# Performance work log

Hardware: AMD Instinct MI355X
Metric: run time of the kernel (lower is better)

The kernel has to match this reference:

```python
import jax, jax.numpy as jnp
import numpy as np

B, SR, D, H, L, NH, ND, E, RK = 64, 29, 768, 3072, 12, 12, 14, 15, 8
S = SR + 1            # cls token + regions
SCALE = 16.0 / 8.0    # lora_alpha / lora_r
NE = L // 2           # number of even (MoE) layers


def _ln(x, g, b, eps):
    m = x.mean(-1, keepdims=True)
    v = ((x - m) ** 2).mean(-1, keepdims=True)
    return (x - m) * jax.lax.rsqrt(v + eps) * g + b


def _ln_plain(x, eps):
    # F.layer_norm with no affine params (expert output norm)
    m = x.mean(-1, keepdims=True)
    v = ((x - m) ** 2).mean(-1, keepdims=True)
    return (x - m) * jax.lax.rsqrt(v + eps)


def _mha(x, Wq, bq, Wk, bk, Wv, bv, Wo, bo):
    b_, s_, _ = x.shape
    dh = D // NH
    q = (x @ Wq.T + bq).reshape(b_, s_, NH, dh)
    k = (x @ Wk.T + bk).reshape(b_, s_, NH, dh)
    v = (x @ Wv.T + bv).reshape(b_, s_, NH, dh)
    att = jax.nn.softmax(jnp.einsum('bqhd,bkhd->bhqk', q, k) / np.float32(np.sqrt(dh)), axis=-1)
    o = jnp.einsum('bhqk,bkhd->bqhd', att, v).reshape(b_, s_, D)
    return o @ Wo.T + bo


def _forward(region_features, mask, cls_token, ln1_g, ln1_b, ln2_g, ln2_b,
             Wq, bq, Wk, bk, Wv, bv, Wao, bao, Wi, bi, Wo, bo, fg, fb,
             cW1, cb1, clng, clnb, cW2, cb2, A_up, B_up, A_down, B_down):
    bsz = region_features.shape[0]
    h = jnp.concatenate([jnp.broadcast_to(cls_token, (bsz, 1, D)), region_features], axis=1)
    col_counts = mask.sum(axis=0)  # [ND], guaranteed > 0 by construction
    for i in range(L):
        n1 = _ln(h, ln1_g[i], ln1_b[i], 1e-12)
        attn = _mha(n1, Wq[i], bq[i], Wk[i], bk[i], Wv[i], bv[i], Wao[i], bao[i])
        res1 = attn + h
        n2 = _ln(res1, ln2_g[i], ln2_b[i], 1e-12)
        inter = jax.nn.gelu(n2 @ Wi[i].T + bi[i], approximate=False)   # [B,S,H]
        base = inter @ Wo[i].T + bo[i]                                  # [B,S,D]
        if i % 2 == 0:
            e = i // 2
            # disease classifier: mask-gather region attention features, mean-pool, per-disease MLP
            region = attn[:, 1:, :]                                     # [B,SR,D]
            pooled = jnp.einsum('rd,brh->bdh', mask, region) / col_counts[None, :, None]
            z = jnp.einsum('bdh,dkh->bdk', pooled, cW1[e]) + cb1[e]
            z = jax.nn.gelu(_ln(z, clng[e], clnb[e], 1e-5), approximate=False)
            preds = jnp.einsum('bdk,dk->bd', z, cW2[e]) + cb2[e]        # [B,ND]
            disease_active = (jax.nn.sigmoid(preds) > 0.5).astype(h.dtype)
            # expert activation: general expert always on; disease experts per region-disease mask
            active = jnp.zeros((bsz, S, E), h.dtype).at[:, :, -1].set(1.0)
            region_active = disease_active[:, None, :] * mask[None, :, :]  # [B,SR,ND]
            active = active.at[:, 1:1 + SR, :ND].set(region_active)
            weights = active / jnp.maximum(active.sum(-1, keepdims=True), 1.0)
            # all 15 LoRA experts densely; zero-weight experts contribute nothing
            lup = jnp.einsum('bser,ehr->bseh', jnp.einsum('bsd,erd->bser', n2, A_up[e]), B_up[e]) * SCALE
            hid = inter[:, :, None, :] + lup                             # [B,S,E,H]
            ldown = jnp.einsum('bser,edr->bsed', jnp.einsum('bseh,erh->bser', hid, A_down[e]), B_down[e]) * SCALE
            out_e = _ln_plain(base[:, :, None, :] + ldown, 1e-5)         # [B,S,E,D]
            ffn_out = jnp.einsum('bsed,bse->bsd', out_e, weights)
        else:
            ffn_out = base
        h = ffn_out + res1
    return _ln(h, fg, fb, 1e-12)


def setup_inputs() -> dict:
    key = jax.random.key(0)
    ks = iter(jax.random.split(key, 64))
    p = lambda *sh: 0.02 * jax.random.normal(next(ks), sh, dtype=jnp.float32)
    g = lambda *sh: 1.0 + 0.02 * jax.random.normal(next(ks), sh, dtype=jnp.float32)
    return dict(
        region_features=jax.random.normal(next(ks), (B, SR, D), dtype=jnp.float32),
        mask=jax.random.bernoulli(next(ks), 0.5, (SR, ND)).astype(jnp.float32).at[0, :].set(1.0),
        cls_token=p(1, 1, D),
        ln1_g=g(L, D), ln1_b=p(L, D), ln2_g=g(L, D), ln2_b=p(L, D),
        Wq=p(L, D, D), bq=p(L, D), Wk=p(L, D, D), bk=p(L, D),
        Wv=p(L, D, D), bv=p(L, D), Wao=p(L, D, D), bao=p(L, D),
        Wi=p(L, H, D), bi=p(L, H), Wo=p(L, D, H), bo=p(L, D),
        fg=g(D), fb=p(D),
        cW1=p(NE, ND, D // 2, D), cb1=p(NE, ND, D // 2),
        clng=g(NE, ND, D // 2), clnb=p(NE, ND, D // 2),
        cW2=p(NE, ND, D // 2), cb2=p(NE, ND),
        A_up=p(NE, E, RK, D), B_up=p(NE, E, H, RK),
        A_down=p(NE, E, RK, H), B_down=p(NE, E, D, RK),
    )


def reference(region_features, mask, cls_token, ln1_g, ln1_b, ln2_g, ln2_b,
              Wq, bq, Wk, bk, Wv, bv, Wao, bao, Wi, bi, Wo, bo, fg, fb,
              cW1, cb1, clng, clnb, cW2, cb2, A_up, B_up, A_down, B_down):
    return _forward(region_features, mask, cls_token, ln1_g, ln1_b, ln2_g, ln2_b,
                    Wq, bq, Wk, bk, Wv, bv, Wao, bao, Wi, bi, Wo, bo, fg, fb,
                    cW1, cb1, clng, clnb, cW2, cb2, A_up, B_up, A_down, B_down)
```

## Files before the change

### kernel.cpp

```cpp
#include <hip/hip_runtime.h>

namespace {

constexpr int kB = 64, kSR = 29, kS = 30, kD = 768, kH = 3072, kL = 12;
constexpr int kNH = 12, kND = 14, kE = 15, kNE = 6;
constexpr int kRows = kB * kS;
constexpr int kQKV = 2304;

typedef __attribute__((ext_vector_type(8))) short s16x8;
typedef __attribute__((ext_vector_type(4))) float fx4;

__device__ __forceinline__ float gelu_f(float x) {
  return 0.5f * x * (1.0f + erff(x * 0.70710678118654752f));
}

__device__ __forceinline__ unsigned short f2bf_u(float x) {
  union { float f; unsigned u; } v;
  v.f = x;
  unsigned r = v.u + 0x7fffu + ((v.u >> 16) & 1u);
  return (unsigned short)(r >> 16);
}
__device__ __forceinline__ float bfu2f(unsigned short h) {
  union { unsigned u; float f; } v;
  v.u = ((unsigned)h) << 16;
  return v.f;
}

__device__ __forceinline__ void g2l16(const short* g, short* l) {
  __builtin_amdgcn_global_load_lds(
      (const __attribute__((address_space(1))) unsigned int*)g,
      (__attribute__((address_space(3))) unsigned int*)l, 16, 0, 0);
}

template <int N>
__device__ __forceinline__ void waitcnt_vm() {
  if constexpr (N == 0)
    asm volatile("s_waitcnt vmcnt(0)" ::: "memory");
  else if constexpr (N == 4)
    asm volatile("s_waitcnt vmcnt(4)" ::: "memory");
  else if constexpr (N == 6)
    asm volatile("s_waitcnt vmcnt(6)" ::: "memory");
  else
    asm volatile("s_waitcnt vmcnt(8)" ::: "memory");
  __builtin_amdgcn_sched_barrier(0);
}

__device__ __forceinline__ void swz_block(int& bx, int& by, int& bz) {
  int gx = gridDim.x, gy = gridDim.y;
  int nwg = gx * gy * (int)gridDim.z;
  int orig = blockIdx.x + gx * (blockIdx.y + gy * blockIdx.z);
  int q = nwg >> 3, r = nwg & 7;
  int xcd = orig & 7, idx = orig >> 3;
  int s = (xcd < r ? xcd * (q + 1) : r * (q + 1) + (xcd - r) * q) + idx;
  bx = s % gx;
  int t2 = s / gx;
  by = t2 % gy;
  bz = t2 / gy;
}

__device__ __forceinline__ float block_sum(float v) {
  __shared__ float sb[4];
#pragma unroll
  for (int o = 32; o > 0; o >>= 1) v += __shfl_down(v, o, 64);
  int w = threadIdx.x >> 6;
  __syncthreads();
  if ((threadIdx.x & 63) == 0) sb[w] = v;
  __syncthreads();
  return sb[0] + sb[1] + sb[2] + sb[3];
}

__device__ __forceinline__ float dot8(const float* __restrict__ p,
                                      const float* __restrict__ q) {
  float4 x = *(const float4*)p;
  float4 y = *(const float4*)(p + 4);
  return x.x * q[0] + x.y * q[1] + x.z * q[2] + x.w * q[3] +
         y.x * q[4] + y.y * q[5] + y.z * q[6] + y.w * q[7];
}

template <int BM, int BN, int MODE>
__global__ __launch_bounds__(256) void gemm_hl(
    const short* __restrict__ Ah, const short* __restrict__ Al,
    const short* __restrict__ Bh, const short* __restrict__ Bl,
    const float* __restrict__ bias, float* __restrict__ Cf,
    short* __restrict__ Ch, short* __restrict__ Cl, int K, int ldc, int act,
    int kchunk, long bsA, long bsB, long bsBias, long bsC) {
  constexpr int MFR = BM / 16, NFR = BN / 16;
  constexpr int NA = 2 * MFR, NB = 2 * NFR, LPW = (NA + NB) / 4;
  constexpr int MF_W = MFR / 2, NF_W = NFR / 2;
  constexpr int ABUF = 2 * MFR * 512, BBUF = 2 * NFR * 512;
  __shared__ __align__(16) short As[3][2][MFR][512];
  __shared__ __align__(16) short Bs[3][2][NFR][512];
  int bx, by, bz;
  swz_block(bx, by, bz);
  const int t = threadIdx.x, w = t >> 6, lane = t & 63;
  const int lr = lane & 15, lg = lane >> 4;
  const int m0 = by * BM, n0 = bx * BN;
  const int kst = K >> 5;
  int k0 = 0;
  if (MODE == 1) k0 = bz * kchunk;
  if (MODE == 2) {
    Ah += bz * bsA;
    Al += bz * bsA;
    Bh += bz * bsB;
    Bl += bz * bsB;
    if (bias) bias += bz * bsBias;
    Cf += bz * bsC;
  }
  const int nsteps = (MODE == 1 ? kchunk : K) >> 5;
  const int wmf = (w & 1) * MF_W, wnf = (w >> 1) * NF_W;

  const short* gp[LPW];
  short* lp[LPW];
  int bo[LPW], adv[LPW];
#pragma unroll
  for (int q = 0; q < LPW; q++) {
    int f = w * LPW + q;
    if (f < NA) {
      int p = f & 1, mf = f >> 1;
      gp[q] = (p ? Al : Ah) + (size_t)(m0 + mf * 16 + lr) * K + k0 + lg * 8;
      lp[q] = &As[0][p][mf][0];
      bo[q] = ABUF;
      adv[q] = 32;
    } else {
      int fb = f - NA, p = fb & 1, nf = fb >> 1;
      gp[q] = (p ? Bl : Bh) + ((size_t)(n0 / 16 + nf) * kst + (k0 >> 5)) * 512 +
              lane * 8;
      lp[q] = &Bs[0][p][nf][0];
      bo[q] = BBUF;
      adv[q] = 512;
    }
  }

  auto stage = [&](int bufidx) {
#pragma unroll
    for (int q = 0; q < LPW; q++) {
      g2l16(gp[q], lp[q] + bufidx * bo[q]);
      gp[q] += adv[q];
    }
  };

  fx4 acc[MF_W][NF_W];
#pragma unroll
  for (int i = 0; i < MF_W; i++)
#pragma unroll
    for (int j = 0; j < NF_W; j++) acc[i][j] = (fx4)0.f;

  stage(0);
  stage(1);
  waitcnt_vm<LPW>();
  __builtin_amdgcn_s_barrier();
  __builtin_amdgcn_sched_barrier(0);

  int cur = 0;
  for (int s = 0; s < nsteps; s++) {
    if (s + 2 < nsteps) {
      int nb = cur + 2;
      if (nb >= 3) nb -= 3;
      stage(nb);
    }
    s16x8 af[MF_W][2], bf[NF_W][2];
#pragma unroll
    for (int fm = 0; fm < MF_W; fm++) {
      af[fm][0] = *(const s16x8*)&As[cur][0][wmf + fm][lane * 8];
      af[fm][1] = *(const s16x8*)&As[cur][1][wmf + fm][lane * 8];
    }
#pragma unroll
    for (int fn = 0; fn < NF_W; fn++) {
      bf[fn][0] = *(const s16x8*)&Bs[cur][0][wnf + fn][lane * 8];
      bf[fn][1] = *(const s16x8*)&Bs[cur][1][wnf + fn][lane * 8];
    }
#pragma unroll
    for (int fm = 0; fm < MF_W; fm++)
#pragma unroll
      for (int fn = 0; fn < NF_W; fn++)
        acc[fm][fn] = __builtin_amdgcn_mfma_f32_16x16x32_bf16(
            af[fm][0], bf[fn][0], acc[fm][fn], 0, 0, 0);
#pragma unroll
    for (int fm = 0; fm < MF_W; fm++)
#pragma unroll
      for (int fn = 0; fn < NF_W; fn++)
        acc[fm][fn] = __builtin_amdgcn_mfma_f32_16x16x32_bf16(
            af[fm][0], bf[fn][1], acc[fm][fn], 0, 0, 0);
#pragma unroll
    for (int fm = 0; fm < MF_W; fm++)
#pragma unroll
      for (int fn = 0; fn < NF_W; fn++)
        acc[fm][fn] = __builtin_amdgcn_mfma_f32_16x16x32_bf16(
            af[fm][1], bf[fn][0], acc[fm][fn], 0, 0, 0);
    if (s + 2 < nsteps)
      waitcnt_vm<LPW>();
    else
      waitcnt_vm<0>();
    __builtin_amdgcn_s_barrier();
    __builtin_amdgcn_sched_barrier(0);
    cur = (cur == 2) ? 0 : cur + 1;
  }

  const int orow = (lane >> 4) * 4;
#pragma unroll
  for (int fm = 0; fm < MF_W; fm++) {
#pragma unroll
    for (int fn = 0; fn < NF_W; fn++) {
      int col = n0 + (wnf + fn) * 16 + lr;
      if (MODE == 1) {
#pragma unroll
        for (int j = 0; j < 4; j++) {
          int row = m0 + (wmf + fm) * 16 + orow + j;
          atomicAdd(&Cf[(size_t)row * ldc + col], acc[fm][fn][j]);
        }
      } else {
        float bv = bias ? bias[col] : 0.f;
#pragma unroll
        for (int j = 0; j < 4; j++) {
          int row = m0 + (wmf + fm) * 16 + orow + j;
          float v = acc[fm][fn][j] + bv;
          if (act) v = gelu_f(v);
          size_t idx = (size_t)row * ldc + col;
          if (Cf) Cf[idx] = v;
          if (Ch) {
            unsigned short hb = f2bf_u(v);
            Ch[idx] = (short)hb;
            Cl[idx] = (short)f2bf_u(v - bfu2f(hb));
          }
        }
      }
    }
  }
}

__device__ __forceinline__ void pack_store(const float* src, short* ph,
                                           short* pl, size_t o) {
  float4 a = *(const float4*)src;
  float4 b = *(const float4*)(src + 4);
  float v[8] = {a.x, a.y, a.z, a.w, b.x, b.y, b.z, b.w};
  s16x8 hv, lv;
#pragma unroll
  for (int e = 0; e < 8; e++) {
    unsigned short h = f2bf_u(v[e]);
    hv[e] = (short)h;
    lv[e] = (short)f2bf_u(v[e] - bfu2f(h));
  }
  *(s16x8*)(ph + o) = hv;
  *(s16x8*)(pl + o) = lv;
}

__global__ __launch_bounds__(256) void pack_w_k(const float* __restrict__ W,
                                                short* __restrict__ ph,
                                                short* __restrict__ pl, int K,
                                                int ntiles) {
  int tile = blockIdx.x * 4 + (threadIdx.x >> 6);
  if (tile >= ntiles) return;
  int kst = K >> 5;
  int nf = tile / kst, ks = tile - nf * kst;
  int lane = threadIdx.x & 63;
  int lr = lane & 15, lg = lane >> 4;
  const float* src = W + (size_t)(nf * 16 + lr) * K + ks * 32 + lg * 8;
  pack_store(src, ph, pl, (size_t)tile * 512 + lane * 8);
}

__global__ __launch_bounds__(256) void pack_qkv_k(const float* __restrict__ Wq,
                                                  const float* __restrict__ Wk,
                                                  const float* __restrict__ Wv,
                                                  short* __restrict__ ph,
                                                  short* __restrict__ pl) {
  int tile = blockIdx.x * 4 + (threadIdx.x >> 6);
  if (tile >= 144 * 24) return;
  int nf = tile / 24, ks = tile - nf * 24;
  int lane = threadIdx.x & 63;
  int lr = lane & 15, lg = lane >> 4;
  int row = nf * 16 + lr;
  const float* src;
  if (row < 768)
    src = Wq + (size_t)row * 768;
  else if (row < 1536)
    src = Wk + (size_t)(row - 768) * 768;
  else
    src = Wv + (size_t)(row - 1536) * 768;
  pack_store(src + ks * 32 + lg * 8, ph, pl, (size_t)tile * 512 + lane * 8);
}

__global__ __launch_bounds__(256) void pack_pad_k(const float* __restrict__ W,
                                                  short* __restrict__ ph,
                                                  short* __restrict__ pl,
                                                  int K) {
  int tile = blockIdx.x * 4 + (threadIdx.x >> 6);
  int kst = K >> 5;
  if (tile >= 8 * kst) return;
  int nf = tile / kst, ks = tile - nf * kst;
  int lane = threadIdx.x & 63;
  int lr = lane & 15, lg = lane >> 4;
  int row = nf * 16 + lr;
  size_t o = (size_t)tile * 512 + lane * 8;
  if (row < 120) {
    pack_store(W + (size_t)row * K + ks * 32 + lg * 8, ph, pl, o);
  } else {
    *(s16x8*)(ph + o) = (s16x8)0;
    *(s16x8*)(pl + o) = (s16x8)0;
  }
}

__global__ __launch_bounds__(256) void concat_k(const float* __restrict__ rf,
                                                const float* __restrict__ cls,
                                                float* __restrict__ h) {
  int idx = blockIdx.x * 256 + threadIdx.x;
  if (idx >= kRows * kD) return;
  int d = idx % kD;
  int row = idx / kD;
  int s = row % kS;
  int b = row / kS;
  h[idx] = (s == 0) ? cls[d] : rf[((long)b * kSR + (s - 1)) * kD + d];
}

__global__ void cc_k(const float* __restrict__ mask, float* __restrict__ cc) {
  int d = threadIdx.x;
  if (d < kND) {
    float s = 0.f;
    for (int r = 0; r < kSR; r++) s += mask[r * kND + d];
    cc[d] = s;
  }
}

__global__ __launch_bounds__(256) void mmat_k(const float* __restrict__ Adn,
                                              const float* __restrict__ Bup,
                                              float* __restrict__ Mm) {
  int g = blockIdx.x;
  int t = threadIdx.x;
  int pair = t & 63;
  int quarter = t >> 6;
  int rp = pair >> 3, r = pair & 7;
  const float* ad = Adn + (long)(g * 8 + rp) * kH;
  const float* bu = Bup + (long)g * kH * 8 + r;
  float acc = 0.f;
  for (int hh = quarter * 768; hh < quarter * 768 + 768; hh++)
    acc += ad[hh] * bu[hh * 8];
  __shared__ float red[256];
  red[t] = acc;
  __syncthreads();
  if (t < 64) Mm[g * 64 + pair] = red[t] + red[t + 64] + red[t + 128] + red[t + 192];
}

__global__ __launch_bounds__(256) void ln_bf_k(
    const float* __restrict__ x, const float* __restrict__ c2,
    const float* __restrict__ b2, const float* __restrict__ r2,
    float* __restrict__ hout, const float* __restrict__ g,
    const float* __restrict__ b, short* __restrict__ yh,
    short* __restrict__ yl, float eps) {
  int row = blockIdx.x;
  int t = threadIdx.x;
  long rb = (long)row * kD;
  float v0, v1, v2;
  if (c2) {
    v0 = c2[rb + t] + b2[t] + r2[rb + t];
    v1 = c2[rb + t + 256] + b2[t + 256] + r2[rb + t + 256];
    v2 = c2[rb + t + 512] + b2[t + 512] + r2[rb + t + 512];
    hout[rb + t] = v0;
    hout[rb + t + 256] = v1;
    hout[rb + t + 512] = v2;
  } else {
    v0 = x[rb + t];
    v1 = x[rb + t + 256];
    v2 = x[rb + t + 512];
  }
  float m = block_sum(v0 + v1 + v2) * (1.0f / 768.0f);
  float d0 = v0 - m, d1 = v1 - m, d2 = v2 - m;
  float q = block_sum(d0 * d0 + d1 * d1 + d2 * d2);
  float inv = rsqrtf(q * (1.0f / 768.0f) + eps);
#pragma unroll
  for (int c = 0; c < 3; c++) {
    int tt = t + c * 256;
    float dd = (c == 0 ? d0 : c == 1 ? d1 : d2);
    float val = dd * inv * g[tt] + b[tt];
    unsigned short hb = f2bf_u(val);
    yh[rb + tt] = (short)hb;
    yl[rb + tt] = (short)f2bf_u(val - bfu2f(hb));
  }
}

__global__ __launch_bounds__(256) void ln_row_k(
    const float* __restrict__ c2, const float* __restrict__ b2,
    const float* __restrict__ r2, const float* __restrict__ g,
    const float* __restrict__ b, float* __restrict__ y, float eps) {
  int row = blockIdx.x;
  int t = threadIdx.x;
  long rb = (long)row * kD;
  float v0 = c2[rb + t] + b2[t] + r2[rb + t];
  float v1 = c2[rb + t + 256] + b2[t + 256] + r2[rb + t + 256];
  float v2 = c2[rb + t + 512] + b2[t + 512] + r2[rb + t + 512];
  float m = block_sum(v0 + v1 + v2) * (1.0f / 768.0f);
  float d0 = v0 - m, d1 = v1 - m, d2 = v2 - m;
  float q = block_sum(d0 * d0 + d1 * d1 + d2 * d2);
  float inv = rsqrtf(q * (1.0f / 768.0f) + eps);
  y[rb + t] = d0 * inv * g[t] + b[t];
  y[rb + t + 256] = d1 * inv * g[t + 256] + b[t + 256];
  y[rb + t + 512] = d2 * inv * g[t + 512] + b[t + 512];
}

__global__ __launch_bounds__(256) void addln_bf_k(
    const float* __restrict__ a, const float* __restrict__ abias,
    const float* __restrict__ hh, const float* __restrict__ g,
    const float* __restrict__ b, float* __restrict__ r1,
    short* __restrict__ n2h, short* __restrict__ n2l, float eps) {
  int row = blockIdx.x;
  int t = threadIdx.x;
  long rb = (long)row * kD;
  float v0 = a[rb + t] + abias[t] + hh[rb + t];
  float v1 = a[rb + t + 256] + abias[t + 256] + hh[rb + t + 256];
  float v2 = a[rb + t + 512] + abias[t + 512] + hh[rb + t + 512];
  r1[rb + t] = v0;
  r1[rb + t + 256] = v1;
  r1[rb + t + 512] = v2;
  float m = block_sum(v0 + v1 + v2) * (1.0f / 768.0f);
  float d0 = v0 - m, d1 = v1 - m, d2 = v2 - m;
  float q = block_sum(d0 * d0 + d1 * d1 + d2 * d2);
  float inv = rsqrtf(q * (1.0f / 768.0f) + eps);
#pragma unroll
  for (int c = 0; c < 3; c++) {
    int tt = t + c * 256;
    float dd = (c == 0 ? d0 : c == 1 ? d1 : d2);
    float val = dd * inv * g[tt] + b[tt];
    unsigned short hb = f2bf_u(val);
    n2h[rb + tt] = (short)hb;
    n2l[rb + tt] = (short)f2bf_u(val - bfu2f(hb));
  }
}

__global__ __launch_bounds__(256) void attn_k(const float* __restrict__ qkv,
                                              const float* __restrict__ bq,
                                              const float* __restrict__ bk,
                                              const float* __restrict__ bv,
                                              short* __restrict__ oh,
                                              short* __restrict__ ol) {
  int blk = blockIdx.x;
  int b = blk / kNH, hh = blk % kNH;
  __shared__ float qs[30][65], ks[30][65], vs[30][65], ps[30][32];
  int t = threadIdx.x;
  long ibase = (long)b * kS * kQKV + hh * 64;
  long obase = (long)b * kS * kD + hh * 64;
  for (int idx = t; idx < 1920; idx += 256) {
    int s = idx >> 6, d = idx & 63;
    long a = ibase + (long)s * kQKV + d;
    int bcol = hh * 64 + d;
    qs[s][d] = qkv[a] + bq[bcol];
    ks[s][d] = qkv[a + 768] + bk[bcol];
    vs[s][d] = qkv[a + 1536] + bv[bcol];
  }
  __syncthreads();
  for (int idx = t; idx < 900; idx += 256) {
    int r = idx / 30, c = idx % 30;
    float acc = 0.f;
#pragma unroll
    for (int d = 0; d < 64; d++) acc += qs[r][d] * ks[c][d];
    ps[r][c] = acc * 0.125f;
  }
  __syncthreads();
  if (t < 30) {
    float mx = -1e30f;
#pragma unroll
    for (int c = 0; c < 30; c++) mx = fmaxf(mx, ps[t][c]);
    float sm = 0.f;
#pragma unroll
    for (int c = 0; c < 30; c++) sm += expf(ps[t][c] - mx);
    float inv = 1.0f / sm;
#pragma unroll
    for (int c = 0; c < 30; c++) ps[t][c] = expf(ps[t][c] - mx) * inv;
  }
  __syncthreads();
  for (int idx = t; idx < 1920; idx += 256) {
    int r = idx >> 6, d = idx & 63;
    float acc = 0.f;
#pragma unroll
    for (int c = 0; c < 30; c++) acc += ps[r][c] * vs[c][d];
    long a = obase + (long)r * kD + d;
    unsigned short hb = f2bf_u(acc);
    oh[a] = (short)hb;
    ol[a] = (short)f2bf_u(acc - bfu2f(hb));
  }
}

__global__ __launch_bounds__(256) void pool_k(const float* __restrict__ ao,
                                              const float* __restrict__ bao,
                                              const float* __restrict__ mask,
                                              const float* __restrict__ cc,
                                              short* __restrict__ ph,
                                              short* __restrict__ pl) {
  int blk = blockIdx.x;
  int d = blk >> 6, b = blk & 63;
  __shared__ float mr[32];
  int t = threadIdx.x;
  if (t < kSR) mr[t] = mask[t * kND + d];
  __syncthreads();
  float inv = 1.0f / cc[d];
  for (int hd = t; hd < kD; hd += 256) {
    float acc = 0.f;
    for (int r = 0; r < kSR; r++) acc += mr[r] * ao[((long)b * kS + 1 + r) * kD + hd];
    float v = acc * inv + bao[hd];
    unsigned short hb = f2bf_u(v);
    size_t o = (size_t)blk * kD + hd;
    ph[o] = (short)hb;
    pl[o] = (short)f2bf_u(v - bfu2f(hb));
  }
}

__global__ __launch_bounds__(256) void cls2_k(const float* __restrict__ z,
                                              const float* __restrict__ lng,
                                              const float* __restrict__ lnb,
                                              const float* __restrict__ w2,
                                              const float* __restrict__ b2,
                                              float* __restrict__ da) {
  int blk = blockIdx.x;
  int d = blk >> 6, b = blk & 63;
  int t = threadIdx.x;
  const float* zr = z + (long)blk * 384;
  float v0 = zr[t];
  float v1 = (t < 128) ? zr[256 + t] : 0.f;
  float m = block_sum(v0 + v1) * (1.0f / 384.0f);
  float d0 = v0 - m;
  float d1 = (t < 128) ? v1 - m : 0.f;
  float q = block_sum(d0 * d0 + d1 * d1);
  float inv = rsqrtf(q * (1.0f / 384.0f) + 1e-5f);
  const float* lg = lng + (long)d * 384;
  const float* lb = lnb + (long)d * 384;
  const float* wd = w2 + (long)d * 384;
  float p = gelu_f(d0 * inv * lg[t] + lb[t]) * wd[t];
  if (t < 128) p += gelu_f(d1 * inv * lg[256 + t] + lb[256 + t]) * wd[256 + t];
  float ps = block_sum(p);
  if (t == 0) da[b * kND + d] = (ps + b2[d] > 0.f) ? 1.f : 0.f;
}

__global__ __launch_bounds__(256) void vcomb_k(const float* __restrict__ u,
                                               const float* __restrict__ ia,
                                               const float* __restrict__ Mm,
                                               float* __restrict__ vv) {
  int idx = blockIdx.x * 256 + threadIdx.x;
  if (idx >= kRows * 120) return;
  int row = idx / 120, c = idx % 120;
  int e = c >> 3, rp = c & 7;
  const float* Me = Mm + e * 64 + rp * 8;
  const float* ur = u + (long)row * 128 + e * 8;
  float acc = ia[(long)row * 128 + c];
#pragma unroll
  for (int r = 0; r < 8; r++) acc += 2.0f * Me[r] * ur[r];
  vv[(long)row * 128 + c] = acc;
}

__global__ __launch_bounds__(256) void finaleven_k(
    const float* __restrict__ cwo, const float* __restrict__ bo,
    const float* __restrict__ res1, const float* __restrict__ vv,
    const float* __restrict__ Bd, const float* __restrict__ da,
    const float* __restrict__ mask, float* __restrict__ h) {
  int row = blockIdx.x;
  int b = row / kS, s = row % kS;
  int t = threadIdx.x;
  __shared__ float w[16];
  __shared__ float vvs[120];
  if (t < 120) vvs[t] = vv[(long)row * 128 + t];
  if (t < kND) w[t] = (s >= 1) ? da[b * kND + t] * mask[(s - 1) * kND + t] : 0.f;
  if (t == kND) w[kND] = 1.f;
  __syncthreads();
  float wsum = 0.f;
#pragma unroll
  for (int e = 0; e < kE; e++) wsum += w[e];
  float winv = 1.0f / wsum;
  long rb = (long)row * kD;
  float b0 = cwo[rb + t] + bo[t];
  float b1 = cwo[rb + t + 256] + bo[t + 256];
  float b2v = cwo[rb + t + 512] + bo[t + 512];
  float a0 = 0.f, a1 = 0.f, a2 = 0.f;
  for (int e = 0; e < kE; e++) {
    float we = w[e];
    if (we == 0.f) continue;
    const float* vr = vvs + e * 8;
    float y0 = b0 + 2.0f * dot8(Bd + ((long)(e * kD + t)) * 8, vr);
    float y1 = b1 + 2.0f * dot8(Bd + ((long)(e * kD + t + 256)) * 8, vr);
    float y2 = b2v + 2.0f * dot8(Bd + ((long)(e * kD + t + 512)) * 8, vr);
    float m = block_sum(y0 + y1 + y2) * (1.0f / 768.0f);
    float d0 = y0 - m, d1 = y1 - m, d2 = y2 - m;
    float q = block_sum(d0 * d0 + d1 * d1 + d2 * d2);
    float inv = rsqrtf(q * (1.0f / 768.0f) + 1e-5f);
    float sc = we * winv * inv;
    a0 += sc * d0;
    a1 += sc * d1;
    a2 += sc * d2;
  }
  h[rb + t] = a0 + res1[rb + t];
  h[rb + t + 256] = a1 + res1[rb + t + 256];
  h[rb + t + 512] = a2 + res1[rb + t + 512];
}

}

extern "C" void kernel_launch(void* const* d_in, const int* in_sizes, int n_in,
                              void* d_out, int out_size, void* d_ws, size_t ws_size,
                              hipStream_t stream) {
  const float* region = (const float*)d_in[0];
  const float* mask = (const float*)d_in[1];
  const float* cls = (const float*)d_in[2];
  const float* ln1g = (const float*)d_in[3];
  const float* ln1b = (const float*)d_in[4];
  const float* ln2g = (const float*)d_in[5];
  const float* ln2b = (const float*)d_in[6];
  const float* Wq = (const float*)d_in[7];
  const float* bq = (const float*)d_in[8];
  const float* Wk = (const float*)d_in[9];
  const float* bk = (const float*)d_in[10];
  const float* Wv = (const float*)d_in[11];
  const float* bv = (const float*)d_in[12];
  const float* Wao = (const float*)d_in[13];
  const float* bao = (const float*)d_in[14];
  const float* Wi = (const float*)d_in[15];
  const float* bi = (const float*)d_in[16];
  const float* Wo = (const float*)d_in[17];
  const float* bo = (const float*)d_in[18];
  const float* fg = (const float*)d_in[19];
  const float* fb = (const float*)d_in[20];
  const float* cW1 = (const float*)d_in[21];
  const float* cb1 = (const float*)d_in[22];
  const float* clng = (const float*)d_in[23];
  const float* clnb = (const float*)d_in[24];
  const float* cW2 = (const float*)d_in[25];
  const float* cb2 = (const float*)d_in[26];
  const float* Aup = (const float*)d_in[27];
  const float* Bup = (const float*)d_in[28];
  const float* Adn = (const float*)d_in[29];
  const float* Bdn = (const float*)d_in[30];
  float* out = (float*)d_out;

  char* wsb = (char*)d_ws;
  size_t off = 0;
  auto alloc = [&](size_t bytes) {
    char* p = wsb + off;
    off = (off + bytes + 255) & ~(size_t)255;
    return (void*)p;
  };
  float* h = (float*)alloc((size_t)kRows * kD * 4);
  float* qkv = (float*)alloc((size_t)kRows * kQKV * 4);
  float* ao = (float*)alloc((size_t)kRows * kD * 4);
  float* res1 = (float*)alloc((size_t)kRows * kD * 4);
  float* cwo = (float*)alloc((size_t)kRows * kD * 4);
  float* zb = (float*)alloc((size_t)kND * kB * 384 * 4);
  float* da = (float*)alloc((size_t)kB * kND * 4);
  float* ub = (float*)alloc((size_t)kRows * 128 * 4);
  float* ia = (float*)alloc((size_t)kRows * 128 * 4);
  float* vvb = (float*)alloc((size_t)kRows * 128 * 4);
  float* Mm = (float*)alloc((size_t)kNE * kE * 64 * 4);
  float* cc = (float*)alloc(64);
  short* n1h = (short*)alloc((size_t)kRows * kD * 2);
  short* n1l = (short*)alloc((size_t)kRows * kD * 2);
  short* n2h = (short*)alloc((size_t)kRows * kD * 2);
  short* n2l = (short*)alloc((size_t)kRows * kD * 2);
  short* inth = (short*)alloc((size_t)kRows * kH * 2);
  short* intl = (short*)alloc((size_t)kRows * kH * 2);
  short* pooledh = (short*)alloc((size_t)kND * kB * kD * 2);
  short* pooledl = (short*)alloc((size_t)kND * kB * kD * 2);
  short* qkvph = (short*)alloc((size_t)144 * 24 * 512 * 2);
  short* qkvpl = (short*)alloc((size_t)144 * 24 * 512 * 2);
  short* waoph = (short*)alloc((size_t)48 * 24 * 512 * 2);
  short* waopl = (short*)alloc((size_t)48 * 24 * 512 * 2);
  short* wiph = (short*)alloc((size_t)192 * 24 * 512 * 2);
  short* wipl = (short*)alloc((size_t)192 * 24 * 512 * 2);
  short* woph = (short*)alloc((size_t)48 * 96 * 512 * 2);
  short* wopl = (short*)alloc((size_t)48 * 96 * 512 * 2);
  short* luph = (short*)alloc((size_t)8 * 24 * 512 * 2);
  short* lupl = (short*)alloc((size_t)8 * 24 * 512 * 2);
  short* ldph = (short*)alloc((size_t)8 * 96 * 512 * 2);
  short* ldpl = (short*)alloc((size_t)8 * 96 * 512 * 2);
  short* cw1ph = (short*)alloc((size_t)336 * 24 * 512 * 2);
  short* cw1pl = (short*)alloc((size_t)336 * 24 * 512 * 2);

  concat_k<<<(kRows * kD + 255) / 256, 256, 0, stream>>>(region, cls, h);
  cc_k<<<1, 32, 0, stream>>>(mask, cc);
  mmat_k<<<kNE * kE, 256, 0, stream>>>(Adn, Bup, Mm);

  const int nDD = kD * kD;
  const int nDH = kD * kH;

  ln_bf_k<<<kRows, 256, 0, stream>>>(h, nullptr, nullptr, nullptr, nullptr, ln1g,
                                     ln1b, n1h, n1l, 1e-12f);

  for (int i = 0; i < kL; i++) {
    int le = i >> 1;
    bool even = (i % 2) == 0;
    pack_qkv_k<<<(144 * 24) / 4, 256, 0, stream>>>(
        Wq + (long)i * nDD, Wk + (long)i * nDD, Wv + (long)i * nDD, qkvph, qkvpl);
    pack_w_k<<<(48 * 24) / 4, 256, 0, stream>>>(Wao + (long)i * nDD, waoph, waopl,
                                                768, 48 * 24);
    pack_w_k<<<(192 * 24) / 4, 256, 0, stream>>>(Wi + (long)i * nDH, wiph, wipl,
                                                 768, 192 * 24);
    pack_w_k<<<(48 * 96) / 4, 256, 0, stream>>>(Wo + (long)i * nDH, woph, wopl,
                                                3072, 48 * 96);

    gemm_hl<128, 64, 0><<<dim3(36, 15), 256, 0, stream>>>(
        n1h, n1l, qkvph, qkvpl, nullptr, qkv, nullptr, nullptr, 768, kQKV, 0, 0,
        0, 0, 0, 0);
    attn_k<<<kB * kNH, 256, 0, stream>>>(qkv, bq + i * kD, bk + i * kD,
                                         bv + i * kD, n1h, n1l);
    hipMemsetAsync(ao, 0, (size_t)kRows * kD * 4, stream);
    gemm_hl<128, 64, 1><<<dim3(12, 15, 2), 256, 0, stream>>>(
        n1h, n1l, waoph, waopl, nullptr, ao, nullptr, nullptr, 768, kD, 0, 384,
        0, 0, 0, 0);
    addln_bf_k<<<kRows, 256, 0, stream>>>(ao, bao + i * kD, h, ln2g + i * kD,
                                          ln2b + i * kD, res1, n2h, n2l, 1e-12f);
    gemm_hl<128, 64, 0><<<dim3(48, 15), 256, 0, stream>>>(
        n2h, n2l, wiph, wipl, bi + i * kH, nullptr, inth, intl, 768, kH, 1, 0,
        0, 0, 0, 0);
    hipMemsetAsync(cwo, 0, (size_t)kRows * kD * 4, stream);
    gemm_hl<128, 64, 1><<<dim3(12, 15, 4), 256, 0, stream>>>(
        inth, intl, woph, wopl, nullptr, cwo, nullptr, nullptr, 3072, kD, 0, 768,
        0, 0, 0, 0);
    if (even) {
      pack_pad_k<<<(8 * 24 + 3) / 4, 256, 0, stream>>>(
          Aup + (long)le * kE * 8 * kD, luph, lupl, 768);
      pack_pad_k<<<(8 * 96) / 4, 256, 0, stream>>>(
          Adn + (long)le * kE * 8 * kH, ldph, ldpl, 3072);
      pack_w_k<<<(336 * 24) / 4, 256, 0, stream>>>(
          cW1 + (long)le * kND * 384 * kD, cw1ph, cw1pl, 768, 336 * 24);
      hipMemsetAsync(ub, 0, (size_t)kRows * 128 * 4, stream);
      hipMemsetAsync(ia, 0, (size_t)kRows * 128 * 4, stream);
      gemm_hl<128, 64, 1><<<dim3(2, 15, 8), 256, 0, stream>>>(
          n2h, n2l, luph, lupl, nullptr, ub, nullptr, nullptr, 768, 128, 0, 96,
          0, 0, 0, 0);
      gemm_hl<128, 64, 1><<<dim3(2, 15, 16), 256, 0, stream>>>(
          inth, intl, ldph, ldpl, nullptr, ia, nullptr, nullptr, 3072, 128, 0,
          192, 0, 0, 0, 0);
      pool_k<<<kND * kB, 256, 0, stream>>>(ao, bao + i * kD, mask, cc, pooledh,
                                           pooledl);
      gemm_hl<64, 64, 2><<<dim3(6, 1, 14), 256, 0, stream>>>(
          pooledh, pooledl, cw1ph, cw1pl, cb1 + (long)le * kND * 384, zb,
          nullptr, nullptr, 768, 384, 0, 0, (long)64 * kD, (long)576 * 512, 384,
          (long)64 * 384);
      cls2_k<<<kND * kB, 256, 0, stream>>>(zb, clng + (long)le * kND * 384,
                                           clnb + (long)le * kND * 384,
                                           cW2 + (long)le * kND * 384,
                                           cb2 + le * kND, da);
      vcomb_k<<<(kRows * 120 + 255) / 256, 256, 0, stream>>>(
          ub, ia, Mm + le * kE * 64, vvb);
      finaleven_k<<<kRows, 256, 0, stream>>>(cwo, bo + i * kD, res1, vvb,
                                             Bdn + (long)le * kE * kD * 8, da,
                                             mask, h);
      ln_bf_k<<<kRows, 256, 0, stream>>>(h, nullptr, nullptr, nullptr, nullptr,
                                         ln1g + (i + 1) * kD, ln1b + (i + 1) * kD,
                                         n1h, n1l, 1e-12f);
    } else if (i < kL - 1) {
      ln_bf_k<<<kRows, 256, 0, stream>>>(nullptr, cwo, bo + i * kD, res1, h,
                                         ln1g + (i + 1) * kD, ln1b + (i + 1) * kD,
                                         n1h, n1l, 1e-12f);
    } else {
      ln_row_k<<<kRows, 256, 0, stream>>>(cwo, bo + i * kD, res1, fg, fb, out,
                                          1e-12f);
    }
  }
}
```

Before: 3.262 ms.

## Replace split-K atomics with partial buffers, widen GEMM tiles, fuse packs and layernorm

Split-K GEMMs now write each K-chunk to its own partial buffer with plain stores instead of atomicAdd into a zeroed output. Consumers (layernorm, pooling, vcomb, finaleven) sum the partials, which removes the memsets and atomic contention. GEMM tiles widen from 128x64 to 128x128, the four per-layer weight-pack kernels merge into one launch, and the next layer's LN1 is fused into finaleven_k. The cost is extra partial-buffer memory traffic, and the wider tiles launch fewer blocks.

```diff
diff --git a/kernel.cpp b/kernel.cpp
--- a/kernel.cpp
+++ b/kernel.cpp
@@ -6,6 +6,8 @@
 constexpr int kNH = 12, kND = 14, kE = 15, kNE = 6;
 constexpr int kRows = kB * kS;
 constexpr int kQKV = 2304;
+constexpr long kPS = (long)kRows * kD;
+constexpr long kPSL = (long)kRows * 128;
 
 typedef __attribute__((ext_vector_type(8))) short s16x8;
 typedef __attribute__((ext_vector_type(4))) float fx4;
@@ -97,7 +99,10 @@
   const int m0 = by * BM, n0 = bx * BN;
   const int kst = K >> 5;
   int k0 = 0;
-  if (MODE == 1) k0 = bz * kchunk;
+  if (MODE == 1) {
+    k0 = bz * kchunk;
+    Cf += bz * bsC;
+  }
   if (MODE == 2) {
     Ah += bz * bsA;
     Al += bz * bsA;
@@ -206,7 +211,7 @@
 #pragma unroll
         for (int j = 0; j < 4; j++) {
           int row = m0 + (wmf + fm) * 16 + orow + j;
-          atomicAdd(&Cf[(size_t)row * ldc + col], acc[fm][fn][j]);
+          Cf[(size_t)row * ldc + col] = acc[fm][fn][j];
         }
       } else {
         float bv = bias ? bias[col] : 0.f;
@@ -244,6 +249,49 @@
   *(s16x8*)(pl + o) = lv;
 }
 
+__global__ __launch_bounds__(256) void pack_layer_k(
+    const float* __restrict__ Wq, const float* __restrict__ Wk,
+    const float* __restrict__ Wv, const float* __restrict__ Wao,
+    const float* __restrict__ Wi, const float* __restrict__ Wo,
+    short* __restrict__ qph, short* __restrict__ qpl, short* __restrict__ aph,
+    short* __restrict__ apl, short* __restrict__ iph, short* __restrict__ ipl,
+    short* __restrict__ oph, short* __restrict__ opl) {
+  int tile = blockIdx.x * 4 + (threadIdx.x >> 6);
+  int lane = threadIdx.x & 63;
+  int lr = lane & 15, lg = lane >> 4;
+  const float* src;
+  short *ph, *pl;
+  size_t o;
+  if (tile < 3456) {
+    int nf = tile / 24, ks = tile % 24;
+    int row = nf * 16 + lr;
+    const float* W = row < 768 ? Wq : row < 1536 ? Wk : Wv;
+    int r = row < 768 ? row : row < 1536 ? row - 768 : row - 1536;
+    src = W + (size_t)r * 768 + ks * 32 + lg * 8;
+    ph = qph; pl = qpl;
+    o = (size_t)tile * 512 + lane * 8;
+  } else if (tile < 4608) {
+    int idx = tile - 3456;
+    int nf = idx / 24, ks = idx % 24;
+    src = Wao + (size_t)(nf * 16 + lr) * 768 + ks * 32 + lg * 8;
+    ph = aph; pl = apl;
+    o = (size_t)idx * 512 + lane * 8;
+  } else if (tile < 9216) {
+    int idx = tile - 4608;
+    int nf = idx / 24, ks = idx % 24;
+    src = Wi + (size_t)(nf * 16 + lr) * 768 + ks * 32 + lg * 8;
+    ph = iph; pl = ipl;
+    o = (size_t)idx * 512 + lane * 8;
+  } else {
+    int idx = tile - 9216;
+    int nf = idx / 96, ks = idx % 96;
+    src = Wo + (size_t)(nf * 16 + lr) * 3072 + ks * 32 + lg * 8;
+    ph = oph; pl = opl;
+    o = (size_t)idx * 512 + lane * 8;
+  }
+  pack_store(src, ph, pl, o);
+}
+
 __global__ __launch_bounds__(256) void pack_w_k(const float* __restrict__ W,
                                                 short* __restrict__ ph,
                                                 short* __restrict__ pl, int K,
@@ -256,27 +304,6 @@
   int lr = lane & 15, lg = lane >> 4;
   const float* src = W + (size_t)(nf * 16 + lr) * K + ks * 32 + lg * 8;
   pack_store(src, ph, pl, (size_t)tile * 512 + lane * 8);
-}
-
-__global__ __launch_bounds__(256) void pack_qkv_k(const float* __restrict__ Wq,
-                                                  const float* __restrict__ Wk,
-                                                  const float* __restrict__ Wv,
-                                                  short* __restrict__ ph,
-                                                  short* __restrict__ pl) {
-  int tile = blockIdx.x * 4 + (threadIdx.x >> 6);
-  if (tile >= 144 * 24) return;
-  int nf = tile / 24, ks = tile - nf * 24;
-  int lane = threadIdx.x & 63;
-  int lr = lane & 15, lg = lane >> 4;
-  int row = nf * 16 + lr;
-  const float* src;
-  if (row < 768)
-    src = Wq + (size_t)row * 768;
-  else if (row < 1536)
-    src = Wk + (size_t)(row - 768) * 768;
-  else
-    src = Wv + (size_t)(row - 1536) * 768;
-  pack_store(src + ks * 32 + lg * 8, ph, pl, (size_t)tile * 512 + lane * 8);
 }
 
 __global__ __launch_bounds__(256) void pack_pad_k(const float* __restrict__ W,
@@ -339,28 +366,16 @@
   if (t < 64) Mm[g * 64 + pair] = red[t] + red[t + 64] + red[t + 128] + red[t + 192];
 }
 
-__global__ __launch_bounds__(256) void ln_bf_k(
-    const float* __restrict__ x, const float* __restrict__ c2,
-    const float* __restrict__ b2, const float* __restrict__ r2,
-    float* __restrict__ hout, const float* __restrict__ g,
-    const float* __restrict__ b, short* __restrict__ yh,
-    short* __restrict__ yl, float eps) {
+__global__ __launch_bounds__(256) void ln_bf_k(const float* __restrict__ x,
+                                               const float* __restrict__ g,
+                                               const float* __restrict__ b,
+                                               short* __restrict__ yh,
+                                               short* __restrict__ yl,
+                                               float eps) {
   int row = blockIdx.x;
   int t = threadIdx.x;
   long rb = (long)row * kD;
-  float v0, v1, v2;
-  if (c2) {
-    v0 = c2[rb + t] + b2[t] + r2[rb + t];
-    v1 = c2[rb + t + 256] + b2[t + 256] + r2[rb + t + 256];
-    v2 = c2[rb + t + 512] + b2[t + 512] + r2[rb + t + 512];
-    hout[rb + t] = v0;
-    hout[rb + t + 256] = v1;
-    hout[rb + t + 512] = v2;
-  } else {
-    v0 = x[rb + t];
-    v1 = x[rb + t + 256];
-    v2 = x[rb + t + 512];
-  }
+  float v0 = x[rb + t], v1 = x[rb + t + 256], v2 = x[rb + t + 512];
   float m = block_sum(v0 + v1 + v2) * (1.0f / 768.0f);
   float d0 = v0 - m, d1 = v1 - m, d2 = v2 - m;
   float q = block_sum(d0 * d0 + d1 * d1 + d2 * d2);
@@ -376,16 +391,62 @@
   }
 }
 
+__global__ __launch_bounds__(256) void ln_parts_k(
+    const float* __restrict__ parts, const float* __restrict__ b2,
+    const float* __restrict__ r2, float* __restrict__ hout,
+    const float* __restrict__ g, const float* __restrict__ b,
+    short* __restrict__ yh, short* __restrict__ yl, float eps) {
+  int row = blockIdx.x;
+  int t = threadIdx.x;
+  long rb = (long)row * kD;
+  float v0, v1, v2;
+  {
+    float s0 = 0, s1 = 0, s2 = 0;
+#pragma unroll
+    for (int p = 0; p < 4; p++) {
+      s0 += parts[p * kPS + rb + t];
+      s1 += parts[p * kPS + rb + t + 256];
+      s2 += parts[p * kPS + rb + t + 512];
+    }
+    v0 = s0 + b2[t] + r2[rb + t];
+    v1 = s1 + b2[t + 256] + r2[rb + t + 256];
+    v2 = s2 + b2[t + 512] + r2[rb + t + 512];
+  }
+  hout[rb + t] = v0;
+  hout[rb + t + 256] = v1;
+  hout[rb + t + 512] = v2;
+  float m = block_sum(v0 + v1 + v2) * (1.0f / 768.0f);
+  float d0 = v0 - m, d1 = v1 - m, d2 = v2 - m;
+  float q = block_sum(d0 * d0 + d1 * d1 + d2 * d2);
+  float inv = rsqrtf(q * (1.0f / 768.0f) + eps);
+#pragma unroll
+  for (int c = 0; c < 3; c++) {
+    int tt = t + c * 256;
+    float dd = (c == 0 ? d0 : c == 1 ? d1 : d2);
+    float val = dd * inv * g[tt] + b[tt];
+    unsigned short hb = f2bf_u(val);
+    yh[rb + tt] = (short)hb;
+    yl[rb + tt] = (short)f2bf_u(val - bfu2f(hb));
+  }
+}
+
 __global__ __launch_bounds__(256) void ln_row_k(
-    const float* __restrict__ c2, const float* __restrict__ b2,
+    const float* __restrict__ parts, const float* __restrict__ b2,
     const float* __restrict__ r2, const float* __restrict__ g,
     const float* __restrict__ b, float* __restrict__ y, float eps) {
   int row = blockIdx.x;
   int t = threadIdx.x;
   long rb = (long)row * kD;
-  float v0 = c2[rb + t] + b2[t] + r2[rb + t];
-  float v1 = c2[rb + t + 256] + b2[t + 256] + r2[rb + t + 256];
-  float v2 = c2[rb + t + 512] + b2[t + 512] + r2[rb + t + 512];
+  float s0 = 0, s1 = 0, s2 = 0;
+#pragma unroll
+  for (int p = 0; p < 4; p++) {
+    s0 += parts[p * kPS + rb + t];
+    s1 += parts[p * kPS + rb + t + 256];
+    s2 += parts[p * kPS + rb + t + 512];
+  }
+  float v0 = s0 + b2[t] + r2[rb + t];
+  float v1 = s1 + b2[t + 256] + r2[rb + t + 256];
+  float v2 = s2 + b2[t + 512] + r2[rb + t + 512];
   float m = block_sum(v0 + v1 + v2) * (1.0f / 768.0f);
   float d0 = v0 - m, d1 = v1 - m, d2 = v2 - m;
   float q = block_sum(d0 * d0 + d1 * d1 + d2 * d2);
@@ -396,16 +457,18 @@
 }
 
 __global__ __launch_bounds__(256) void addln_bf_k(
-    const float* __restrict__ a, const float* __restrict__ abias,
+    const float* __restrict__ aparts, const float* __restrict__ abias,
     const float* __restrict__ hh, const float* __restrict__ g,
     const float* __restrict__ b, float* __restrict__ r1,
     short* __restrict__ n2h, short* __restrict__ n2l, float eps) {
   int row = blockIdx.x;
   int t = threadIdx.x;
   long rb = (long)row * kD;
-  float v0 = a[rb + t] + abias[t] + hh[rb + t];
-  float v1 = a[rb + t + 256] + abias[t + 256] + hh[rb + t + 256];
-  float v2 = a[rb + t + 512] + abias[t + 512] + hh[rb + t + 512];
+  float v0 = aparts[rb + t] + aparts[kPS + rb + t] + abias[t] + hh[rb + t];
+  float v1 = aparts[rb + t + 256] + aparts[kPS + rb + t + 256] + abias[t + 256] +
+             hh[rb + t + 256];
+  float v2 = aparts[rb + t + 512] + aparts[kPS + rb + t + 512] + abias[t + 512] +
+             hh[rb + t + 512];
   r1[rb + t] = v0;
   r1[rb + t + 256] = v1;
   r1[rb + t + 512] = v2;
@@ -477,7 +540,7 @@
   }
 }
 
-__global__ __launch_bounds__(256) void pool_k(const float* __restrict__ ao,
+__global__ __launch_bounds__(256) void pool_k(const float* __restrict__ aparts,
                                               const float* __restrict__ bao,
                                               const float* __restrict__ mask,
                                               const float* __restrict__ cc,
@@ -492,7 +555,10 @@
   float inv = 1.0f / cc[d];
   for (int hd = t; hd < kD; hd += 256) {
     float acc = 0.f;
-    for (int r = 0; r < kSR; r++) acc += mr[r] * ao[((long)b * kS + 1 + r) * kD + hd];
+    for (int r = 0; r < kSR; r++) {
+      long o = ((long)b * kS + 1 + r) * kD + hd;
+      acc += mr[r] * (aparts[o] + aparts[kPS + o]);
+    }
     float v = acc * inv + bao[hd];
     unsigned short hb = f2bf_u(v);
     size_t o = (size_t)blk * kD + hd;
@@ -527,8 +593,8 @@
   if (t == 0) da[b * kND + d] = (ps + b2[d] > 0.f) ? 1.f : 0.f;
 }
 
-__global__ __launch_bounds__(256) void vcomb_k(const float* __restrict__ u,
-                                               const float* __restrict__ ia,
+__global__ __launch_bounds__(256) void vcomb_k(const float* __restrict__ ubp,
+                                               const float* __restrict__ iap,
                                                const float* __restrict__ Mm,
                                                float* __restrict__ vv) {
   int idx = blockIdx.x * 256 + threadIdx.x;
@@ -536,18 +602,30 @@
   int row = idx / 120, c = idx % 120;
   int e = c >> 3, rp = c & 7;
   const float* Me = Mm + e * 64 + rp * 8;
-  const float* ur = u + (long)row * 128 + e * 8;
-  float acc = ia[(long)row * 128 + c];
-#pragma unroll
-  for (int r = 0; r < 8; r++) acc += 2.0f * Me[r] * ur[r];
-  vv[(long)row * 128 + c] = acc;
+  long rb = (long)row * 128;
+  float acc = 0.f;
+#pragma unroll
+  for (int p = 0; p < 8; p++) acc += iap[p * kPSL + rb + c];
+  float uv[8];
+#pragma unroll
+  for (int r = 0; r < 8; r++) {
+    float u = 0.f;
+#pragma unroll
+    for (int p = 0; p < 4; p++) u += ubp[p * kPSL + rb + e * 8 + r];
+    uv[r] = u;
+  }
+#pragma unroll
+  for (int r = 0; r < 8; r++) acc += 2.0f * Me[r] * uv[r];
+  vv[rb + c] = acc;
 }
 
 __global__ __launch_bounds__(256) void finaleven_k(
-    const float* __restrict__ cwo, const float* __restrict__ bo,
+    const float* __restrict__ parts, const float* __restrict__ bo,
     const float* __restrict__ res1, const float* __restrict__ vv,
     const float* __restrict__ Bd, const float* __restrict__ da,
-    const float* __restrict__ mask, float* __restrict__ h) {
+    const float* __restrict__ mask, float* __restrict__ h,
+    const float* __restrict__ g1, const float* __restrict__ b1,
+    short* __restrict__ n1h, short* __restrict__ n1l) {
   int row = blockIdx.x;
   int b = row / kS, s = row % kS;
   int t = threadIdx.x;
@@ -562,16 +640,20 @@
   for (int e = 0; e < kE; e++) wsum += w[e];
   float winv = 1.0f / wsum;
   long rb = (long)row * kD;
-  float b0 = cwo[rb + t] + bo[t];
-  float b1 = cwo[rb + t + 256] + bo[t + 256];
-  float b2v = cwo[rb + t + 512] + bo[t + 512];
+  float b0 = bo[t], b1v = bo[t + 256], b2v = bo[t + 512];
+#pragma unroll
+  for (int p = 0; p < 4; p++) {
+    b0 += parts[p * kPS + rb + t];
+    b1v += parts[p * kPS + rb + t + 256];
+    b2v += parts[p * kPS + rb + t + 512];
+  }
   float a0 = 0.f, a1 = 0.f, a2 = 0.f;
   for (int e = 0; e < kE; e++) {
     float we = w[e];
     if (we == 0.f) continue;
     const float* vr = vvs + e * 8;
     float y0 = b0 + 2.0f * dot8(Bd + ((long)(e * kD + t)) * 8, vr);
-    float y1 = b1 + 2.0f * dot8(Bd + ((long)(e * kD + t + 256)) * 8, vr);
+    float y1 = b1v + 2.0f * dot8(Bd + ((long)(e * kD + t + 256)) * 8, vr);
     float y2 = b2v + 2.0f * dot8(Bd + ((long)(e * kD + t + 512)) * 8, vr);
     float m = block_sum(y0 + y1 + y2) * (1.0f / 768.0f);
     float d0 = y0 - m, d1 = y1 - m, d2 = y2 - m;
@@ -582,9 +664,25 @@
     a1 += sc * d1;
     a2 += sc * d2;
   }
-  h[rb + t] = a0 + res1[rb + t];
-  h[rb + t + 256] = a1 + res1[rb + t + 256];
-  h[rb + t + 512] = a2 + res1[rb + t + 512];
+  float v0 = a0 + res1[rb + t];
+  float v1 = a1 + res1[rb + t + 256];
+  float v2 = a2 + res1[rb + t + 512];
+  h[rb + t] = v0;
+  h[rb + t + 256] = v1;
+  h[rb + t + 512] = v2;
+  float m = block_sum(v0 + v1 + v2) * (1.0f / 768.0f);
+  float d0 = v0 - m, d1 = v1 - m, d2 = v2 - m;
+  float q = block_sum(d0 * d0 + d1 * d1 + d2 * d2);
+  float inv = rsqrtf(q * (1.0f / 768.0f) + 1e-12f);
+#pragma unroll
+  for (int c = 0; c < 3; c++) {
+    int tt = t + c * 256;
+    float dd = (c == 0 ? d0 : c == 1 ? d1 : d2);
+    float val = dd * inv * g1[tt] + b1[tt];
+    unsigned short hb = f2bf_u(val);
+    n1h[rb + tt] = (short)hb;
+    n1l[rb + tt] = (short)f2bf_u(val - bfu2f(hb));
+  }
 }
 
 }
@@ -634,13 +732,13 @@
   };
   float* h = (float*)alloc((size_t)kRows * kD * 4);
   float* qkv = (float*)alloc((size_t)kRows * kQKV * 4);
-  float* ao = (float*)alloc((size_t)kRows * kD * 4);
+  float* aop = (float*)alloc((size_t)2 * kRows * kD * 4);
   float* res1 = (float*)alloc((size_t)kRows * kD * 4);
-  float* cwo = (float*)alloc((size_t)kRows * kD * 4);
+  float* cwop = (float*)alloc((size_t)4 * kRows * kD * 4);
   float* zb = (float*)alloc((size_t)kND * kB * 384 * 4);
   float* da = (float*)alloc((size_t)kB * kND * 4);
-  float* ub = (float*)alloc((size_t)kRows * 128 * 4);
-  float* ia = (float*)alloc((size_t)kRows * 128 * 4);
+  float* ubp = (float*)alloc((size_t)4 * kRows * 128 * 4);
+  float* iap = (float*)alloc((size_t)8 * kRows * 128 * 4);
   float* vvb = (float*)alloc((size_t)kRows * 128 * 4);
   float* Mm = (float*)alloc((size_t)kNE * kE * 64 * 4);
   float* cc = (float*)alloc(64);
@@ -674,55 +772,46 @@
   const int nDD = kD * kD;
   const int nDH = kD * kH;
 
-  ln_bf_k<<<kRows, 256, 0, stream>>>(h, nullptr, nullptr, nullptr, nullptr, ln1g,
-                                     ln1b, n1h, n1l, 1e-12f);
+  ln_bf_k<<<kRows, 256, 0, stream>>>(h, ln1g, ln1b, n1h, n1l, 1e-12f);
 
   for (int i = 0; i < kL; i++) {
     int le = i >> 1;
     bool even = (i % 2) == 0;
-    pack_qkv_k<<<(144 * 24) / 4, 256, 0, stream>>>(
-        Wq + (long)i * nDD, Wk + (long)i * nDD, Wv + (long)i * nDD, qkvph, qkvpl);
-    pack_w_k<<<(48 * 24) / 4, 256, 0, stream>>>(Wao + (long)i * nDD, waoph, waopl,
-                                                768, 48 * 24);
-    pack_w_k<<<(192 * 24) / 4, 256, 0, stream>>>(Wi + (long)i * nDH, wiph, wipl,
-                                                 768, 192 * 24);
-    pack_w_k<<<(48 * 96) / 4, 256, 0, stream>>>(Wo + (long)i * nDH, woph, wopl,
-                                                3072, 48 * 96);
-
-    gemm_hl<128, 64, 0><<<dim3(36, 15), 256, 0, stream>>>(
+    pack_layer_k<<<3456, 256, 0, stream>>>(
+        Wq + (long)i * nDD, Wk + (long)i * nDD, Wv + (long)i * nDD,
+        Wao + (long)i * nDD, Wi + (long)i * nDH, Wo + (long)i * nDH, qkvph,
+        qkvpl, waoph, waopl, wiph, wipl, woph, wopl);
+
+    gemm_hl<128, 128, 0><<<dim3(18, 15), 256, 0, stream>>>(
         n1h, n1l, qkvph, qkvpl, nullptr, qkv, nullptr, nullptr, 768, kQKV, 0, 0,
         0, 0, 0, 0);
     attn_k<<<kB * kNH, 256, 0, stream>>>(qkv, bq + i * kD, bk + i * kD,
                                          bv + i * kD, n1h, n1l);
-    hipMemsetAsync(ao, 0, (size_t)kRows * kD * 4, stream);
-    gemm_hl<128, 64, 1><<<dim3(12, 15, 2), 256, 0, stream>>>(
-        n1h, n1l, waoph, waopl, nullptr, ao, nullptr, nullptr, 768, kD, 0, 384,
-        0, 0, 0, 0);
-    addln_bf_k<<<kRows, 256, 0, stream>>>(ao, bao + i * kD, h, ln2g + i * kD,
+    gemm_hl<128, 128, 1><<<dim3(6, 15, 2), 256, 0, stream>>>(
+        n1h, n1l, waoph, waopl, nullptr, aop, nullptr, nullptr, 768, kD, 0, 384,
+        0, 0, 0, kPS);
+    addln_bf_k<<<kRows, 256, 0, stream>>>(aop, bao + i * kD, h, ln2g + i * kD,
                                           ln2b + i * kD, res1, n2h, n2l, 1e-12f);
-    gemm_hl<128, 64, 0><<<dim3(48, 15), 256, 0, stream>>>(
+    gemm_hl<128, 128, 0><<<dim3(24, 15), 256, 0, stream>>>(
         n2h, n2l, wiph, wipl, bi + i * kH, nullptr, inth, intl, 768, kH, 1, 0,
         0, 0, 0, 0);
-    hipMemsetAsync(cwo, 0, (size_t)kRows * kD * 4, stream);
-    gemm_hl<128, 64, 1><<<dim3(12, 15, 4), 256, 0, stream>>>(
-        inth, intl, woph, wopl, nullptr, cwo, nullptr, nullptr, 3072, kD, 0, 768,
-        0, 0, 0, 0);
+    gemm_hl<128, 128, 1><<<dim3(6, 15, 4), 256, 0, stream>>>(
+        inth, intl, woph, wopl, nullptr, cwop, nullptr, nullptr, 3072, kD, 0,
+        768, 0, 0, 0, kPS);
     if (even) {
-      pack_pad_k<<<(8 * 24 + 3) / 4, 256, 0, stream>>>(
-          Aup + (long)le * kE * 8 * kD, luph, lupl, 768);
-      pack_pad_k<<<(8 * 96) / 4, 256, 0, stream>>>(
-          Adn + (long)le * kE * 8 * kH, ldph, ldpl, 3072);
+      pack_pad_k<<<48, 256, 0, stream>>>(Aup + (long)le * kE * 8 * kD, luph,
+                                         lupl, 768);
+      pack_pad_k<<<192, 256, 0, stream>>>(Adn + (long)le * kE * 8 * kH, ldph,
+                                          ldpl, 3072);
       pack_w_k<<<(336 * 24) / 4, 256, 0, stream>>>(
           cW1 + (long)le * kND * 384 * kD, cw1ph, cw1pl, 768, 336 * 24);
-      hipMemsetAsync(ub, 0, (size_t)kRows * 128 * 4, stream);
-      hipMemsetAsync(ia, 0, (size_t)kRows * 128 * 4, stream);
-      gemm_hl<128, 64, 1><<<dim3(2, 15, 8), 256, 0, stream>>>(
-          n2h, n2l, luph, lupl, nullptr, ub, nullptr, nullptr, 768, 128, 0, 96,
-          0, 0, 0, 0);
-      gemm_hl<128, 64, 1><<<dim3(2, 15, 16), 256, 0, stream>>>(
-          inth, intl, ldph, ldpl, nullptr, ia, nullptr, nullptr, 3072, 128, 0,
-          192, 0, 0, 0, 0);
-      pool_k<<<kND * kB, 256, 0, stream>>>(ao, bao + i * kD, mask, cc, pooledh,
+      gemm_hl<128, 128, 1><<<dim3(1, 15, 4), 256, 0, stream>>>(
+          n2h, n2l, luph, lupl, nullptr, ubp, nullptr, nullptr, 768, 128, 0, 192,
+          0, 0, 0, kPSL);
+      gemm_hl<128, 128, 1><<<dim3(1, 15, 8), 256, 0, stream>>>(
+          inth, intl, ldph, ldpl, nullptr, iap, nullptr, nullptr, 3072, 128, 0,
+          384, 0, 0, 0, kPSL);
+      pool_k<<<kND * kB, 256, 0, stream>>>(aop, bao + i * kD, mask, cc, pooledh,
                                            pooledl);
       gemm_hl<64, 64, 2><<<dim3(6, 1, 14), 256, 0, stream>>>(
           pooledh, pooledl, cw1ph, cw1pl, cb1 + (long)le * kND * 384, zb,
@@ -733,19 +822,17 @@
                                            cW2 + (long)le * kND * 384,
                                            cb2 + le * kND, da);
       vcomb_k<<<(kRows * 120 + 255) / 256, 256, 0, stream>>>(
-          ub, ia, Mm + le * kE * 64, vvb);
-      finaleven_k<<<kRows, 256, 0, stream>>>(cwo, bo + i * kD, res1, vvb,
-                                             Bdn + (long)le * kE * kD * 8, da,
-                                             mask, h);
-      ln_bf_k<<<kRows, 256, 0, stream>>>(h, nullptr, nullptr, nullptr, nullptr,
-                                         ln1g + (i + 1) * kD, ln1b + (i + 1) * kD,
-                                         n1h, n1l, 1e-12f);
+          ubp, iap, Mm + le * kE * 64, vvb);
+      finaleven_k<<<kRows, 256, 0, stream>>>(
+          cwop, bo + i * kD, res1, vvb, Bdn + (long)le * kE * kD * 8, da, mask,
+          h, ln1g + (i + 1) * kD, ln1b + (i + 1) * kD, n1h, n1l);
     } else if (i < kL - 1) {
-      ln_bf_k<<<kRows, 256, 0, stream>>>(nullptr, cwo, bo + i * kD, res1, h,
-                                         ln1g + (i + 1) * kD, ln1b + (i + 1) * kD,
-                                         n1h, n1l, 1e-12f);
+      ln_parts_k<<<kRows, 256, 0, stream>>>(cwop, bo + i * kD, res1, h,
+                                            ln1g + (i + 1) * kD,
+                                            ln1b + (i + 1) * kD, n1h, n1l,
+                                            1e-12f);
     } else {
-      ln_row_k<<<kRows, 256, 0, stream>>>(cwo, bo + i * kD, res1, fg, fb, out,
+      ln_row_k<<<kRows, 256, 0, stream>>>(cwop, bo + i * kD, res1, fg, fb, out,
                                           1e-12f);
     }
   }
```

After: 3.269 ms. No clear change (+0.2%).
